# Optimization experiments

Measured on AMD Instinct MI355X. Metric: run time of the kernel, lower is better.

Reference implementation:

```python
import jax, jax.numpy as jnp
import numpy as np
import math

# 4th-order Gauss-Legendre RK Butcher tableau
_SQRT3 = math.sqrt(3.0)
A11, A12 = 0.25, 0.25 - _SQRT3 / 6.0
A21, A22 = 0.25 + _SQRT3 / 6.0, 0.25
B1, B2 = 0.5, 0.5


def setup_inputs() -> dict:
    key = jax.random.key(0)
    k1, k2, k3, k4 = jax.random.split(key, 4)
    B, D = 8192, 64
    # scale matrices so I - h*a*A stays well-conditioned
    A1 = jax.random.normal(k1, (B, D, D), dtype=jnp.float32) * 0.1
    A2 = jax.random.normal(k2, (B, D, D), dtype=jnp.float32) * 0.1
    y0 = jax.random.normal(k3, (B, D), dtype=jnp.float32)
    h = jax.random.uniform(k4, (), dtype=jnp.float32) * 0.1 + 0.01
    return {"A1": A1, "A2": A2, "y0": y0, "h": h}


def reference(A1, A2, y0, h):
    # A1, A2: (B, d, d) = A(t0 + c1*h), A(t0 + c2*h); y0: (B, d); h: scalar
    d = y0.shape[-1]
    I = jnp.eye(d, dtype=y0.dtype)
    # assemble 2x2 block system L K = R  (same layout as the torch slice writes)
    top = jnp.concatenate([I - h * A11 * A1, -h * A12 * A1], axis=-1)  # (B, d, 2d)
    bot = jnp.concatenate([-h * A21 * A2, I - h * A22 * A2], axis=-1)  # (B, d, 2d)
    L = jnp.concatenate([top, bot], axis=-2)                            # (B, 2d, 2d)
    R1 = jnp.einsum('bij,bj->bi', A1, y0)
    R2 = jnp.einsum('bij,bj->bi', A2, y0)
    R = jnp.concatenate([R1, R2], axis=-1)                              # (B, 2d)
    K = jnp.linalg.solve(L, R[..., None])[..., 0]                       # (B, 2d)
    k1, k2 = K[..., :d], K[..., d:]
    y_next = y0 + h * (B1 * k1 + B2 * k2)
    return y_next, jnp.stack((A1, A2), axis=0)
```

## Files before the change

kernel.cpp:

```cpp
#include <hip/hip_runtime.h>

#define D    64
#define NIT  8
#define WPB  4

#define CA11 0.25f
#define CA12 -0.038675134594812866f
#define CA21 0.5386751345948129f
#define CA22 0.25f

__global__ __launch_bounds__(256, 3) void glrk_kernel(
    const float* __restrict__ A1, const float* __restrict__ A2,
    const float* __restrict__ y0, const float* __restrict__ hp,
    float* __restrict__ outy, float* __restrict__ oA1, float* __restrict__ oA2,
    int Btot)
{
    const int wave = threadIdx.x >> 6;
    const int lane = threadIdx.x & 63;
    const int b    = blockIdx.x * WPB + wave;
    if (b >= Btot) return;

    __shared__ float sT[WPB][D * 32];
    __shared__ float sV[WPB][2][D];

    const float  h    = *hp;
    const size_t moff = (size_t)b * (D * D);
    const float  y    = y0[(size_t)b * D + lane];

    float4 rowA[16], rowB[16];
    float* tile = sT[wave];

    auto stage = [&](const float* __restrict__ src, float* __restrict__ dst, float4* row) {
        const float4* s4 = (const float4*)(src + moff);
        float4*       d4 = (float4*)(dst + moff);
#pragma unroll
        for (int g = 0; g < 2; ++g) {
            float4 tmp[8];
#pragma unroll
            for (int j = 0; j < 8; ++j) {
                const int r  = j * 8 + (lane >> 3);
                const int i4 = r * 16 + 8 * g + (lane & 7);
                tmp[j] = s4[i4];
                d4[i4] = tmp[j];
            }
            const int pw = ((lane & 7) ^ (lane >> 3)) * 4 + (lane >> 3) * 32;
#pragma unroll
            for (int j = 0; j < 8; ++j)
                *(float4*)&tile[pw + j * 256] = tmp[j];
            __builtin_amdgcn_wave_barrier();
#pragma unroll
            for (int c = 0; c < 8; ++c) {
                const int p = c ^ (lane & 7);
                row[8 * g + c] = *(const float4*)&tile[lane * 32 + p * 4];
            }
            __builtin_amdgcn_wave_barrier();
        }
    };
    stage(A1, oA1, rowA);
    stage(A2, oA2, rowB);

    float k1 = 0.f, k2 = 0.f;
    float* v1 = sV[wave][0];
    float* v2 = sV[wave][1];
    const float4* v14 = (const float4*)v1;
    const float4* v24 = (const float4*)v2;

#pragma unroll 1
    for (int it = 0; it < NIT; ++it) {
        v1[lane] = fmaf(h, fmaf(CA11, k1, CA12 * k2), y);
        __builtin_amdgcn_wave_barrier();
        float a0 = 0.f, a1 = 0.f, a2 = 0.f, a3 = 0.f;
#pragma unroll
        for (int c = 0; c < 16; ++c) {
            const float4 u = v14[c];
            a0 = fmaf(rowA[c].x, u.x, a0);
            a1 = fmaf(rowA[c].y, u.y, a1);
            a2 = fmaf(rowA[c].z, u.z, a2);
            a3 = fmaf(rowA[c].w, u.w, a3);
        }
        k1 = (a0 + a1) + (a2 + a3);

        v2[lane] = fmaf(h, fmaf(CA21, k1, CA22 * k2), y);
        __builtin_amdgcn_wave_barrier();
        float b0 = 0.f, b1 = 0.f, b2 = 0.f, b3 = 0.f;
#pragma unroll
        for (int c = 0; c < 16; ++c) {
            const float4 u = v24[c];
            b0 = fmaf(rowB[c].x, u.x, b0);
            b1 = fmaf(rowB[c].y, u.y, b1);
            b2 = fmaf(rowB[c].z, u.z, b2);
            b3 = fmaf(rowB[c].w, u.w, b3);
        }
        k2 = (b0 + b1) + (b2 + b3);
    }

    outy[(size_t)b * D + lane] = fmaf(h, 0.5f * (k1 + k2), y);
}

extern "C" void kernel_launch(void* const* d_in, const int* in_sizes, int n_in,
                              void* d_out, int out_size, void* d_ws, size_t ws_size,
                              hipStream_t stream) {
    const float* A1 = (const float*)d_in[0];
    const float* A2 = (const float*)d_in[1];
    const float* y0 = (const float*)d_in[2];
    const float* hp = (const float*)d_in[3];

    const int B = in_sizes[2] / D;

    float* outy = (float*)d_out;
    float* oA1  = outy + (size_t)B * D;
    float* oA2  = oA1 + (size_t)B * D * D;

    const int grid = (B + WPB - 1) / WPB;
    glrk_kernel<<<grid, 64 * WPB, 0, stream>>>(A1, A2, y0, hp, outy, oA1, oA2, B);
}
```

Before: 449.0 us.

## Use persistent single-wave blocks with async global-to-LDS prefetch of next batch

Replaces one-wave-per-batch blocks with a persistent grid of 1024 single-wave blocks that loop over batch elements. Each block issues direct global-to-LDS loads for the next batch's A1/A2 matrices while running the fixed-point iterations on the current one, so memory latency overlaps compute. The A1/A2 copy-out is now read back from the swizzled LDS buffers. This uses 32KB+ of LDS per single-wave block, which limits occupancy and makes correctness depend on the hand-written vmcnt/lgkmcnt waits.

Result: no change. 454.3 us (+1.2%).

```diff
diff --git a/kernel.cpp b/kernel.cpp
--- a/kernel.cpp
+++ b/kernel.cpp
@@ -2,99 +2,133 @@
 
 #define D    64
 #define NIT  8
-#define WPB  4
+#define GRID 1024
 
 #define CA11 0.25f
 #define CA12 -0.038675134594812866f
 #define CA21 0.5386751345948129f
 #define CA22 0.25f
 
-__global__ __launch_bounds__(256, 3) void glrk_kernel(
+typedef const __attribute__((address_space(1))) void* gas_p;
+typedef __attribute__((address_space(3))) void*       las_p;
+
+#define WAIT_VM16()  asm volatile("s_waitcnt vmcnt(16)" ::: "memory")
+#define WAIT_LGKM0() asm volatile("s_waitcnt lgkmcnt(0)" ::: "memory")
+
+__global__ __launch_bounds__(64, 1) void glrk_kernel(
     const float* __restrict__ A1, const float* __restrict__ A2,
     const float* __restrict__ y0, const float* __restrict__ hp,
     float* __restrict__ outy, float* __restrict__ oA1, float* __restrict__ oA2,
     int Btot)
 {
-    const int wave = threadIdx.x >> 6;
-    const int lane = threadIdx.x & 63;
-    const int b    = blockIdx.x * WPB + wave;
-    if (b >= Btot) return;
+    const int lane = threadIdx.x;
 
-    __shared__ float sT[WPB][D * 32];
-    __shared__ float sV[WPB][2][D];
+    __shared__ __align__(16) float P[D * D];
+    __shared__ __align__(16) float Q[D * D];
+    __shared__ __align__(16) float sV[2][D];
 
-    const float  h    = *hp;
-    const size_t moff = (size_t)b * (D * D);
-    const float  y    = y0[(size_t)b * D + lane];
+    const float h = *hp;
+
+    auto dma_matrix = [&](const float* __restrict__ src, float* __restrict__ buf) {
+#pragma unroll
+        for (int j = 0; j < 16; ++j) {
+            const int r  = j * 4 + (lane >> 4);
+            const int f4 = r * 16 + ((lane & 15) ^ (r & 7));
+            __builtin_amdgcn_global_load_lds((gas_p)(src + f4 * 4),
+                                             (las_p)(buf + j * 256), 16, 0, 0);
+        }
+    };
+
+    int b = blockIdx.x;
+    const int stride = gridDim.x;
+    bool have = (b < Btot);
+    if (have) {
+        const size_t m = (size_t)b * (D * D);
+        dma_matrix(A1 + m, P);
+        dma_matrix(A2 + m, Q);
+    }
 
     float4 rowA[16], rowB[16];
-    float* tile = sT[wave];
-
-    auto stage = [&](const float* __restrict__ src, float* __restrict__ dst, float4* row) {
-        const float4* s4 = (const float4*)(src + moff);
-        float4*       d4 = (float4*)(dst + moff);
-#pragma unroll
-        for (int g = 0; g < 2; ++g) {
-            float4 tmp[8];
-#pragma unroll
-            for (int j = 0; j < 8; ++j) {
-                const int r  = j * 8 + (lane >> 3);
-                const int i4 = r * 16 + 8 * g + (lane & 7);
-                tmp[j] = s4[i4];
-                d4[i4] = tmp[j];
-            }
-            const int pw = ((lane & 7) ^ (lane >> 3)) * 4 + (lane >> 3) * 32;
-#pragma unroll
-            for (int j = 0; j < 8; ++j)
-                *(float4*)&tile[pw + j * 256] = tmp[j];
-            __builtin_amdgcn_wave_barrier();
-#pragma unroll
-            for (int c = 0; c < 8; ++c) {
-                const int p = c ^ (lane & 7);
-                row[8 * g + c] = *(const float4*)&tile[lane * 32 + p * 4];
-            }
-            __builtin_amdgcn_wave_barrier();
-        }
-    };
-    stage(A1, oA1, rowA);
-    stage(A2, oA2, rowB);
-
-    float k1 = 0.f, k2 = 0.f;
-    float* v1 = sV[wave][0];
-    float* v2 = sV[wave][1];
-    const float4* v14 = (const float4*)v1;
-    const float4* v24 = (const float4*)v2;
+    const float4* v14 = (const float4*)sV[0];
+    const float4* v24 = (const float4*)sV[1];
 
 #pragma unroll 1
-    for (int it = 0; it < NIT; ++it) {
-        v1[lane] = fmaf(h, fmaf(CA11, k1, CA12 * k2), y);
-        __builtin_amdgcn_wave_barrier();
-        float a0 = 0.f, a1 = 0.f, a2 = 0.f, a3 = 0.f;
+    while (have) {
+        const int    bn        = b + stride;
+        const bool   have_next = (bn < Btot);
+        const size_t m         = (size_t)b * (D * D);
+
+        const float y = y0[(size_t)b * D + lane];
+
+        WAIT_VM16();
 #pragma unroll
-        for (int c = 0; c < 16; ++c) {
-            const float4 u = v14[c];
-            a0 = fmaf(rowA[c].x, u.x, a0);
-            a1 = fmaf(rowA[c].y, u.y, a1);
-            a2 = fmaf(rowA[c].z, u.z, a2);
-            a3 = fmaf(rowA[c].w, u.w, a3);
+        for (int c = 0; c < 16; ++c)
+            rowA[c] = *(const float4*)&P[lane * 64 + ((c ^ (lane & 7)) * 4)];
+        {
+            float4* d4 = (float4*)(oA1 + m);
+#pragma unroll
+            for (int j = 0; j < 16; ++j) {
+                const int s = j * 64 + lane;
+                const int r = s >> 4;
+                d4[s] = *(const float4*)&P[r * 64 + (((s & 15) ^ (r & 7)) * 4)];
+            }
         }
-        k1 = (a0 + a1) + (a2 + a3);
 
-        v2[lane] = fmaf(h, fmaf(CA21, k1, CA22 * k2), y);
-        __builtin_amdgcn_wave_barrier();
-        float b0 = 0.f, b1 = 0.f, b2 = 0.f, b3 = 0.f;
+        WAIT_VM16();
 #pragma unroll
-        for (int c = 0; c < 16; ++c) {
-            const float4 u = v24[c];
-            b0 = fmaf(rowB[c].x, u.x, b0);
-            b1 = fmaf(rowB[c].y, u.y, b1);
-            b2 = fmaf(rowB[c].z, u.z, b2);
-            b3 = fmaf(rowB[c].w, u.w, b3);
+        for (int c = 0; c < 16; ++c)
+            rowB[c] = *(const float4*)&Q[lane * 64 + ((c ^ (lane & 7)) * 4)];
+        {
+            float4* d4 = (float4*)(oA2 + m);
+#pragma unroll
+            for (int j = 0; j < 16; ++j) {
+                const int s = j * 64 + lane;
+                const int r = s >> 4;
+                d4[s] = *(const float4*)&Q[r * 64 + (((s & 15) ^ (r & 7)) * 4)];
+            }
         }
-        k2 = (b0 + b1) + (b2 + b3);
+
+        WAIT_LGKM0();
+        if (have_next) {
+            const size_t mn = (size_t)bn * (D * D);
+            dma_matrix(A1 + mn, P);
+            dma_matrix(A2 + mn, Q);
+        }
+
+        float k1 = 0.f, k2 = 0.f;
+#pragma unroll 1
+        for (int it = 0; it < NIT; ++it) {
+            sV[0][lane] = fmaf(h, fmaf(CA11, k1, CA12 * k2), y);
+            __builtin_amdgcn_wave_barrier();
+            float a0 = 0.f, a1 = 0.f, a2 = 0.f, a3 = 0.f;
+#pragma unroll
+            for (int c = 0; c < 16; ++c) {
+                const float4 u = v14[c];
+                a0 = fmaf(rowA[c].x, u.x, a0);
+                a1 = fmaf(rowA[c].y, u.y, a1);
+                a2 = fmaf(rowA[c].z, u.z, a2);
+                a3 = fmaf(rowA[c].w, u.w, a3);
+            }
+            k1 = (a0 + a1) + (a2 + a3);
+
+            sV[1][lane] = fmaf(h, fmaf(CA21, k1, CA22 * k2), y);
+            __builtin_amdgcn_wave_barrier();
+            float b0 = 0.f, b1 = 0.f, b2 = 0.f, b3 = 0.f;
+#pragma unroll
+            for (int c = 0; c < 16; ++c) {
+                const float4 u = v24[c];
+                b0 = fmaf(rowB[c].x, u.x, b0);
+                b1 = fmaf(rowB[c].y, u.y, b1);
+                b2 = fmaf(rowB[c].z, u.z, b2);
+                b3 = fmaf(rowB[c].w, u.w, b3);
+            }
+            k2 = (b0 + b1) + (b2 + b3);
+        }
+
+        outy[(size_t)b * D + lane] = fmaf(h, 0.5f * (k1 + k2), y);
+
+        b = bn; have = have_next;
     }
-
-    outy[(size_t)b * D + lane] = fmaf(h, 0.5f * (k1 + k2), y);
 }
 
 extern "C" void kernel_launch(void* const* d_in, const int* in_sizes, int n_in,
@@ -111,6 +145,6 @@
     float* oA1  = outy + (size_t)B * D;
     float* oA2  = oA1 + (size_t)B * D * D;
 
-    const int grid = (B + WPB - 1) / WPB;
-    glrk_kernel<<<grid, 64 * WPB, 0, stream>>>(A1, A2, y0, hp, outy, oA1, oA2, B);
+    const int grid = (B < GRID) ? B : GRID;
+    glrk_kernel<<<grid, 64, 0, stream>>>(A1, A2, y0, hp, outy, oA1, oA2, B);
 }
```
